# Kernel optimization log

Hardware: AMD Instinct MI355X
Metric: run time of the kernel (lower is better)

The kernel has to match this reference:

```python
import jax, jax.numpy as jnp
import numpy as np

D_MODEL = 512  # scale uses sqrt(d_model), faithful to source (not sqrt(d_k))


def setup_inputs() -> dict:
    key = jax.random.key(0)
    ks = jax.random.split(key, 9)
    S, H, DK, DV = 4096, 8, 128, 64
    w = lambda k, shape: jax.random.normal(k, shape, jnp.float32) * 0.02
    return {
        "x": jax.random.normal(ks[0], (S, D_MODEL), jnp.float32),
        "Wq": w(ks[1], (H, D_MODEL, DK)), "bq": w(ks[2], (H, DK)),
        "Wk": w(ks[3], (H, D_MODEL, DK)), "bk": w(ks[4], (H, DK)),
        "Wv": w(ks[5], (H, D_MODEL, DV)), "bv": w(ks[6], (H, DV)),
        "Wo": w(ks[7], (H * DV, D_MODEL)), "bo": w(ks[8], (D_MODEL,)),
    }


def reference(x, Wq, bq, Wk, bk, Wv, bv, Wo, bo):
    # Per-head Q/K/V projections, batched over heads: [H, S, dk/dv]
    q = jnp.einsum('sd,hdk->hsk', x, Wq) + bq[:, None, :]
    k = jnp.einsum('sd,hdk->hsk', x, Wk) + bk[:, None, :]
    v = jnp.einsum('sd,hdv->hsv', x, Wv) + bv[:, None, :]
    # scaled dot-product; source divides by sqrt(d_model), mask branch is a no-op
    scores = jnp.einsum('hsk,htk->hst', q, k) / jnp.sqrt(jnp.float32(D_MODEL))
    probs = jax.nn.softmax(scores, axis=-1)  # softmax(dim=1) on 2D == last axis
    heads = jnp.einsum('hst,htv->hsv', probs, v)          # [H, S, DV]
    concat = jnp.transpose(heads, (1, 0, 2)).reshape(x.shape[0], -1)  # [S, H*DV]
    return concat @ Wo + bo
```

## Files before the change

kernel.cpp:

```cpp
#include <hip/hip_runtime.h>
#include <hip/hip_bf16.h>
#include <math.h>

typedef __bf16 bf16_t;
typedef __bf16 bf16x4 __attribute__((ext_vector_type(4)));
typedef __bf16 bf16x8 __attribute__((ext_vector_type(8)));
typedef float  f32x4  __attribute__((ext_vector_type(4)));

#define LOG2E   1.4426950408889634f
#define QSCALE  0.04419417382415922f
#define QS_TOT  (QSCALE * LOG2E)

static __device__ __forceinline__ f32x4 mfma16(bf16x8 a, bf16x8 b, f32x4 c) {
    return __builtin_amdgcn_mfma_f32_16x16x32_bf16(a, b, c, 0, 0, 0);
}

static __device__ __forceinline__ void gload16(void* lds, const void* g) {
    __builtin_amdgcn_global_load_lds(
        (const __attribute__((address_space(1))) unsigned int*)g,
        (__attribute__((address_space(3))) unsigned int*)lds, 16, 0, 0);
}

__global__ void k_stage_all(const float* __restrict__ x,
                            const float* __restrict__ Wq, const float* __restrict__ Wk,
                            const float* __restrict__ Wv, const float* __restrict__ Wo,
                            const float* __restrict__ bq, const float* __restrict__ bk,
                            const float* __restrict__ bv,
                            bf16_t* __restrict__ xb, bf16_t* __restrict__ Wcat,
                            bf16_t* __restrict__ Wot, float* __restrict__ bcat) {
    __shared__ float tl[64][65];
    int b = blockIdx.x;
    if (b < 2048) {
        int i = (b * 256 + (int)threadIdx.x) * 4;
        f32x4 v = *(const f32x4*)(x + i);
        bf16x4 o;
        o[0] = (bf16_t)v[0]; o[1] = (bf16_t)v[1]; o[2] = (bf16_t)v[2]; o[3] = (bf16_t)v[3];
        *(bf16x4*)(xb + i) = o;
        return;
    }
    if (b < 2432) {
        int bb = b - 2048;
        int p = bb >> 7, bid = bb & 127;
        int h = bid >> 4, rem = bid & 15, dt = rem >> 1, ct = rem & 1;
        if (p == 2 && ct) return;
        int cols = (p == 2) ? 64 : 128;
        const float* src = (p == 0 ? Wq : (p == 1 ? Wk : Wv)) + h * 512 * cols;
        int d0 = dt * 64, c0 = ct * 64;
        int cin = threadIdx.x & 63, rb = threadIdx.x >> 6;
        #pragma unroll
        for (int j = 0; j < 16; j++) {
            int dl = rb * 16 + j;
            tl[dl][cin] = src[(d0 + dl) * cols + c0 + cin];
        }
        __syncthreads();
        float sc = (p == 0) ? QS_TOT : 1.0f;
        int nl = threadIdx.x >> 2, dch = (threadIdx.x & 3) * 16;
        int n = h * 320 + p * 128 + c0 + nl;
        bf16_t* dst = Wcat + n * 512 + d0 + dch;
        #pragma unroll
        for (int e = 0; e < 16; e += 4) {
            bf16x4 o;
            #pragma unroll
            for (int q = 0; q < 4; q++) o[q] = (bf16_t)(tl[dch + e + q][nl] * sc);
            *(bf16x4*)(dst + e) = o;
        }
        return;
    }
    if (b < 2496) {
        int bb = b - 2432;
        int r0 = (bb >> 3) * 64, c0 = (bb & 7) * 64;
        int cin = threadIdx.x & 63, rb = threadIdx.x >> 6;
        #pragma unroll
        for (int j = 0; j < 16; j++) {
            int rl = rb * 16 + j;
            tl[rl][cin] = Wo[(r0 + rl) * 512 + c0 + cin];
        }
        __syncthreads();
        int nl = threadIdx.x >> 2, dch = (threadIdx.x & 3) * 16;
        bf16_t* dst = Wot + (c0 + nl) * 512 + r0 + dch;
        #pragma unroll
        for (int e = 0; e < 16; e += 4) {
            bf16x4 o;
            #pragma unroll
            for (int q = 0; q < 4; q++) o[q] = (bf16_t)tl[dch + e + q][nl];
            *(bf16x4*)(dst + e) = o;
        }
        return;
    }
    {
        int n = (b - 2496) * 256 + (int)threadIdx.x;
        if (n >= 2560) return;
        int h = n / 320, r = n % 320;
        float v;
        if (r < 128)      v = bq[h * 128 + r] * QS_TOT;
        else if (r < 256) v = bk[h * 128 + r - 128];
        else              v = bv[h * 64 + r - 256];
        bcat[n] = v;
    }
}

static __device__ __forceinline__ void stage_tile(bf16_t* lds, const bf16_t* src_base,
                                                  int row0, int kk, int wv, int lane) {
    #pragma unroll
    for (int j = 0; j < 2; ++j) {
        int row = j * 64 + wv * 16 + (lane >> 2);
        int slot = lane & 3;
        const bf16_t* src = src_base + (size_t)(row0 + row) * 512 + kk
                          + ((slot ^ ((row >> 1) & 3)) << 3);
        gload16(lds + (j * 64 + wv * 16) * 32, src);
    }
}

__global__ __launch_bounds__(256) void k_gemm_qkv(
        const bf16_t* __restrict__ xb, const bf16_t* __restrict__ Wcat,
        const float* __restrict__ bcat,
        bf16_t* __restrict__ Qb, bf16_t* __restrict__ Kb, bf16_t* __restrict__ Vt) {
    __shared__ __align__(16) bf16_t a_lds[2][128 * 32];
    __shared__ __align__(16) bf16_t b_lds[2][128 * 32];

    int lane = threadIdx.x & 63, wv = threadIdx.x >> 6;
    int qi = lane & 15, g = lane >> 4;
    int m0 = blockIdx.x * 128;
    int n0 = blockIdx.y * 128;

    f32x4 acc[4][4];
    #pragma unroll
    for (int ar = 0; ar < 4; ar++)
        #pragma unroll
        for (int br = 0; br < 4; br++) acc[ar][br] = (f32x4){0.f,0.f,0.f,0.f};

    int arow0 = (wv >> 1) * 64;
    int brow0 = (wv & 1) * 64;

    stage_tile(&a_lds[0][0], xb,   m0, 0, wv, lane);
    stage_tile(&b_lds[0][0], Wcat, n0, 0, wv, lane);

    for (int t = 0; t < 16; ++t) {
        __syncthreads();
        int cur = t & 1;
        if (t + 1 < 16) {
            stage_tile(&a_lds[cur ^ 1][0], xb,   m0, (t + 1) * 32, wv, lane);
            stage_tile(&b_lds[cur ^ 1][0], Wcat, n0, (t + 1) * 32, wv, lane);
        }
        const char* abase = (const char*)&a_lds[cur][0];
        const char* bbase = (const char*)&b_lds[cur][0];
        bf16x8 af[4], bf[4];
        #pragma unroll
        for (int ar = 0; ar < 4; ar++) {
            int row = arow0 + ar * 16 + qi;
            af[ar] = *(const bf16x8*)(abase + row * 64 + (((g ^ (row >> 1)) & 3) << 4));
        }
        #pragma unroll
        for (int br = 0; br < 4; br++) {
            int row = brow0 + br * 16 + qi;
            bf[br] = *(const bf16x8*)(bbase + row * 64 + (((g ^ (row >> 1)) & 3) << 4));
        }
        __builtin_amdgcn_s_setprio(1);
        #pragma unroll
        for (int ar = 0; ar < 4; ar++)
            #pragma unroll
            for (int br = 0; br < 4; br++)
                acc[ar][br] = mfma16(af[ar], bf[br], acc[ar][br]);
        __builtin_amdgcn_s_setprio(0);
    }

    int mrow = m0 + arow0;
    int ncol = n0 + brow0;
    #pragma unroll
    for (int br = 0; br < 4; br++) {
        int n = ncol + br * 16 + qi;
        float bias = bcat[n];
        int h = n / 320, r = n % 320;
        #pragma unroll
        for (int ar = 0; ar < 4; ar++)
            #pragma unroll
            for (int i = 0; i < 4; i++) {
                int rr = mrow + ar * 16 + g * 4 + i;
                float val = acc[ar][br][i] + bias;
                if (r < 128)      Qb[(h * 4096 + rr) * 128 + r]         = (bf16_t)val;
                else if (r < 256) Kb[(h * 4096 + rr) * 128 + (r - 128)] = (bf16_t)val;
                else {
                    int cp = (rr & ~31) | (((rr >> 2) & 3) << 3) | (((rr >> 4) & 1) << 2) | (rr & 3);
                    Vt[(h * 64 + (r - 256)) * 4096 + cp] = (bf16_t)val;
                }
            }
    }
}

static __device__ __forceinline__ void stage_k(bf16_t* kbuf, const bf16_t* Kh,
                                               int kt, int wv, int lane) {
    #pragma unroll
    for (int j = 0; j < 4; ++j) {
        int local = wv * 16 + j * 4 + (lane >> 4);
        int physcol = (lane & 15) << 4;
        const char* src = (const char*)(Kh + (size_t)(kt + local) * 128)
                        + (physcol ^ ((local & 7) << 4));
        gload16(kbuf + (wv * 16 + j * 4) * 128, src);
    }
}

static __device__ __forceinline__ void stage_v(bf16_t* vbuf, const bf16_t* Vh,
                                               int kt, int wv, int lane) {
    #pragma unroll
    for (int jj = 0; jj < 2; ++jj) {
        int j = wv * 2 + jj;
        int dv = j * 8 + (lane >> 3);
        int slot = lane & 7;
        const bf16_t* src = Vh + (size_t)dv * 4096 + kt + ((slot ^ (dv & 7)) << 3);
        gload16(vbuf + j * 512, src);
    }
}

__global__ __launch_bounds__(256) void k_attn(
        const bf16_t* __restrict__ Qb, const bf16_t* __restrict__ Kb,
        const bf16_t* __restrict__ Vt, bf16_t* __restrict__ Cb,
        float* __restrict__ Opart, float* __restrict__ Lpart) {
    __shared__ __align__(16) bf16_t k_lds[2][64 * 128];
    __shared__ __align__(16) bf16_t v_lds[3][64 * 64];

    const int lane = threadIdx.x & 63, wv = threadIdx.x >> 6;
    const int qi = lane & 15, g = lane >> 4;

    int nwg = 32 * 8 * gridDim.z, cpx = nwg >> 3;
    int wgid = blockIdx.x + 32 * (blockIdx.y + 8 * blockIdx.z);
    int wk = (wgid & 7) * cpx + (wgid >> 3);
    const int qb = wk & 31, h = (wk >> 5) & 7, split = wk >> 8;

    const int nsplits = gridDim.z;
    const int tbase = 64 / nsplits, trem = 64 % nsplits;
    const int tstart = split * tbase + (split < trem ? split : trem);
    const int ntiles = tbase + (split < trem ? 1 : 0);

    const int q0 = qb * 128 + wv * 32;
    int rot = (int)(((unsigned)wgid * 2654435761u) >> 24) % ntiles;

    const bf16_t* Qh = Qb + h * 4096 * 128;
    const bf16_t* Kh = Kb + h * 4096 * 128;
    const bf16_t* Vh = Vt + h * 64 * 4096;

    bf16x8 qf[2][4];
    #pragma unroll
    for (int qt = 0; qt < 2; qt++)
        #pragma unroll
        for (int c = 0; c < 4; c++)
            qf[qt][c] = *(const bf16x8*)(Qh + (q0 + qt * 16 + qi) * 128 + c * 32 + g * 8);

    bf16x8 vones;
    #pragma unroll
    for (int e = 0; e < 8; e++) vones[e] = (bf16_t)1.0f;

    f32x4 oacc[2][4], lacc[2];
    #pragma unroll
    for (int qt = 0; qt < 2; qt++) {
        #pragma unroll
        for (int c = 0; c < 4; c++) oacc[qt][c] = (f32x4){0.f,0.f,0.f,0.f};
        lacc[qt] = (f32x4){0.f,0.f,0.f,0.f};
    }

    bf16x8 pbp[2][2];

    {
        int kt0 = (tstart + rot) * 64;
        stage_k(&k_lds[0][0], Kh, kt0, wv, lane);
        stage_v(&v_lds[0][0], Vh, kt0, wv, lane);
    }
    __syncthreads();

    int bc = 0;
    for (int ii = 0; ii < ntiles; ++ii) {
        const int kcur = ii & 1;
        int bn = bc + 1; if (bn == 3) bn = 0;
        int bp = bn + 1; if (bp == 3) bp = 0;

        if (ii + 1 < ntiles) {
            int idn = ii + 1 + rot; if (idn >= ntiles) idn -= ntiles;
            int ktn = (tstart + idn) * 64;
            stage_k(&k_lds[kcur ^ 1][0], Kh, ktn, wv, lane);
            stage_v(&v_lds[bn][0], Vh, ktn, wv, lane);
        }

        f32x4 s[2][4];
        #pragma unroll
        for (int qt = 0; qt < 2; qt++)
            #pragma unroll
            for (int t = 0; t < 4; t++) s[qt][t] = (f32x4){0.f,0.f,0.f,0.f};
        __builtin_amdgcn_s_setprio(1);
        #pragma unroll
        for (int t = 0; t < 4; t++) {
            const bf16_t* kr = &k_lds[kcur][(t * 16 + qi) * 128];
            #pragma unroll
            for (int c = 0; c < 4; c++) {
                int offb = (c * 64 + g * 16) ^ ((qi & 7) << 4);
                bf16x8 kf = *(const bf16x8*)(kr + (offb >> 1));
                s[0][t] = mfma16(kf, qf[0][c], s[0][t]);
                s[1][t] = mfma16(kf, qf[1][c], s[1][t]);
            }
        }

        if (ii > 0) {
            #pragma unroll
            for (int c = 0; c < 4; c++) {
                const char* vrow = (const char*)&v_lds[bp][0] + (c * 16 + qi) * 128;
                #pragma unroll
                for (int u = 0; u < 2; u++) {
                    int offb = (g * 16 + u * 64) ^ ((qi & 7) << 4);
                    bf16x8 vf = *(const bf16x8*)(vrow + offb);
                    oacc[0][c] = mfma16(vf, pbp[0][u], oacc[0][c]);
                    oacc[1][c] = mfma16(vf, pbp[1][u], oacc[1][c]);
                }
            }
            #pragma unroll
            for (int u = 0; u < 2; u++) {
                lacc[0] = mfma16(vones, pbp[0][u], lacc[0]);
                lacc[1] = mfma16(vones, pbp[1][u], lacc[1]);
            }
        }
        __builtin_amdgcn_s_setprio(0);

        float p[2][4][4];
        #pragma unroll
        for (int qt = 0; qt < 2; qt++)
            #pragma unroll
            for (int t = 0; t < 4; t++)
                #pragma unroll
                for (int i = 0; i < 4; i++)
                    p[qt][t][i] = __builtin_amdgcn_exp2f(s[qt][t][i]);

        #pragma unroll
        for (int qt = 0; qt < 2; qt++)
            #pragma unroll
            for (int u = 0; u < 2; u++) {
                bf16x8 t8;
                #pragma unroll
                for (int e = 0; e < 4; e++) {
                    t8[e]     = (bf16_t)p[qt][2 * u][e];
                    t8[4 + e] = (bf16_t)p[qt][2 * u + 1][e];
                }
                pbp[qt][u] = t8;
            }

        bc = bn;
        __syncthreads();
    }

    {
        int bl = bc + 2; if (bl >= 3) bl -= 3;
        __builtin_amdgcn_s_setprio(1);
        #pragma unroll
        for (int c = 0; c < 4; c++) {
            const char* vrow = (const char*)&v_lds[bl][0] + (c * 16 + qi) * 128;
            #pragma unroll
            for (int u = 0; u < 2; u++) {
                int offb = (g * 16 + u * 64) ^ ((qi & 7) << 4);
                bf16x8 vf = *(const bf16x8*)(vrow + offb);
                oacc[0][c] = mfma16(vf, pbp[0][u], oacc[0][c]);
                oacc[1][c] = mfma16(vf, pbp[1][u], oacc[1][c]);
            }
        }
        #pragma unroll
        for (int u = 0; u < 2; u++) {
            lacc[0] = mfma16(vones, pbp[0][u], lacc[0]);
            lacc[1] = mfma16(vones, pbp[1][u], lacc[1]);
        }
        __builtin_amdgcn_s_setprio(0);
    }

    float l[2] = { lacc[0][0], lacc[1][0] };

    if (gridDim.z == 1) {
        #pragma unroll
        for (int qt = 0; qt < 2; qt++) {
            float inv = 1.0f / l[qt];
            int q = q0 + qt * 16 + qi;
            #pragma unroll
            for (int c = 0; c < 4; c++) {
                bf16x4 o4;
                #pragma unroll
                for (int i = 0; i < 4; i++) o4[i] = (bf16_t)(oacc[qt][c][i] * inv);
                *(bf16x4*)(Cb + q * 512 + h * 64 + c * 16 + g * 4) = o4;
            }
        }
    } else {
        #pragma unroll
        for (int qt = 0; qt < 2; qt++) {
            int q = q0 + qt * 16 + qi;
            float* Op = Opart + ((size_t)(split * 8 + h) * 4096 + q) * 64;
            #pragma unroll
            for (int c = 0; c < 4; c++)
                *(f32x4*)(Op + c * 16 + g * 4) = oacc[qt][c];
            if (g == 0)
                Lpart[(size_t)(split * 8 + h) * 4096 + q] = l[qt];
        }
    }
}

__global__ void k_merge(const float* __restrict__ Opart, const float* __restrict__ Lpart,
                        bf16_t* __restrict__ Cb, int splits) {
    int idx = blockIdx.x * 256 + threadIdx.x;
    int q = idx >> 7, rem = idx & 127;
    int hv4 = rem * 4;
    int h = hv4 >> 6, dv = hv4 & 63;

    f32x4 acc = {0.f, 0.f, 0.f, 0.f};
    float L = 0.f;
    for (int s = 0; s < splits; s++) {
        L += Lpart[(size_t)(s * 8 + h) * 4096 + q];
        f32x4 ov = *(const f32x4*)(Opart + ((size_t)(s * 8 + h) * 4096 + q) * 64 + dv);
        #pragma unroll
        for (int e = 0; e < 4; e++) acc[e] += ov[e];
    }
    float inv = 1.0f / L;
    bf16x4 o4;
    #pragma unroll
    for (int e = 0; e < 4; e++) o4[e] = (bf16_t)(acc[e] * inv);
    *(bf16x4*)(Cb + (size_t)q * 512 + hv4) = o4;
}

__global__ __launch_bounds__(256) void k_gemm_out(
        const bf16_t* __restrict__ Cb, const bf16_t* __restrict__ Wot,
        const float* __restrict__ bo, float* __restrict__ out) {
    __shared__ __align__(16) bf16_t a_lds[2][128 * 32];
    __shared__ __align__(16) bf16_t b_lds[2][128 * 32];

    int lane = threadIdx.x & 63, wv = threadIdx.x >> 6;
    int qi = lane & 15, g = lane >> 4;
    int m0 = blockIdx.x * 128;
    int n0 = blockIdx.y * 128;

    f32x4 acc[4][4];
    #pragma unroll
    for (int ar = 0; ar < 4; ar++)
        #pragma unroll
        for (int br = 0; br < 4; br++) acc[ar][br] = (f32x4){0.f,0.f,0.f,0.f};

    int arow0 = (wv >> 1) * 64;
    int brow0 = (wv & 1) * 64;

    stage_tile(&a_lds[0][0], Cb,  m0, 0, wv, lane);
    stage_tile(&b_lds[0][0], Wot, n0, 0, wv, lane);

    for (int t = 0; t < 16; ++t) {
        __syncthreads();
        int cur = t & 1;
        if (t + 1 < 16) {
            stage_tile(&a_lds[cur ^ 1][0], Cb,  m0, (t + 1) * 32, wv, lane);
            stage_tile(&b_lds[cur ^ 1][0], Wot, n0, (t + 1) * 32, wv, lane);
        }
        const char* abase = (const char*)&a_lds[cur][0];
        const char* bbase = (const char*)&b_lds[cur][0];
        bf16x8 af[4], bf[4];
        #pragma unroll
        for (int ar = 0; ar < 4; ar++) {
            int row = arow0 + ar * 16 + qi;
            af[ar] = *(const bf16x8*)(abase + row * 64 + (((g ^ (row >> 1)) & 3) << 4));
        }
        #pragma unroll
        for (int br = 0; br < 4; br++) {
            int row = brow0 + br * 16 + qi;
            bf[br] = *(const bf16x8*)(bbase + row * 64 + (((g ^ (row >> 1)) & 3) << 4));
        }
        __builtin_amdgcn_s_setprio(1);
        #pragma unroll
        for (int ar = 0; ar < 4; ar++)
            #pragma unroll
            for (int br = 0; br < 4; br++)
                acc[ar][br] = mfma16(af[ar], bf[br], acc[ar][br]);
        __builtin_amdgcn_s_setprio(0);
    }

    int mrow = m0 + arow0;
    int ncol = n0 + brow0;
    #pragma unroll
    for (int br = 0; br < 4; br++) {
        int n = ncol + br * 16 + qi;
        float bias = bo[n];
        #pragma unroll
        for (int ar = 0; ar < 4; ar++)
            #pragma unroll
            for (int i = 0; i < 4; i++)
                out[(mrow + ar * 16 + g * 4 + i) * 512 + n] = acc[ar][br][i] + bias;
    }
}

extern "C" void kernel_launch(void* const* d_in, const int* in_sizes, int n_in,
                              void* d_out, int out_size, void* d_ws, size_t ws_size,
                              hipStream_t stream) {
    const float* x  = (const float*)d_in[0];
    const float* Wq = (const float*)d_in[1];
    const float* bq = (const float*)d_in[2];
    const float* Wk = (const float*)d_in[3];
    const float* bk = (const float*)d_in[4];
    const float* Wv = (const float*)d_in[5];
    const float* bv = (const float*)d_in[6];
    const float* Wo = (const float*)d_in[7];
    const float* bo = (const float*)d_in[8];
    float* out = (float*)d_out;

    char* ws = (char*)d_ws;
    bf16_t* xb    = (bf16_t*)(ws + 0);
    bf16_t* Wcat  = (bf16_t*)(ws + 4194304);
    bf16_t* Qb    = (bf16_t*)(ws + 6815744);
    bf16_t* Kb    = (bf16_t*)(ws + 15204352);
    bf16_t* Vt    = (bf16_t*)(ws + 23592960);
    bf16_t* Cb    = (bf16_t*)(ws + 27787264);
    bf16_t* Wot   = (bf16_t*)(ws + 31981568);
    float*  bcat  = (float*)(ws + 32505856);
    float*  Opart = (float*)(ws + 32516096);
    float*  Lprt  = (float*)(ws + 49293312);
    const size_t NEED2 = 49555456;
    int splits = (ws_size >= NEED2) ? 2 : 1;

    hipLaunchKernelGGL(k_stage_all,  dim3(2506),   dim3(256), 0, stream,
                       x, Wq, Wk, Wv, Wo, bq, bk, bv, xb, Wcat, Wot, bcat);
    hipLaunchKernelGGL(k_gemm_qkv,   dim3(32, 20), dim3(256), 0, stream, xb, Wcat, bcat, Qb, Kb, Vt);
    hipLaunchKernelGGL(k_attn,       dim3(32, 8, splits), dim3(256), 0, stream, Qb, Kb, Vt, Cb, Opart, Lprt);
    if (splits > 1)
        hipLaunchKernelGGL(k_merge,  dim3(2048),   dim3(256), 0, stream, Opart, Lprt, Cb, splits);
    hipLaunchKernelGGL(k_gemm_out,   dim3(32, 4),  dim3(256), 0, stream, Cb, Wot, bo, out);
}
```

Before: 105.7 us.

## Restructure attention loop to defer softmax exp into next iteration with ping-pong score buffers

The main attention loop now keeps raw scores in two alternating register sets (sA/sB) and unrolls by two. The exp2/bf16 conversion of the previous tile's scores moves into the next iteration, after the current QK^T MFMAs and just before the PV MFMAs. This lets transcendental work overlap with MFMA latency, and the compiler can schedule across a static buffer swap. In exchange it holds more fp32 registers live, which may raise register pressure or lower occupancy, and it enlarges the code.

```diff
diff --git a/kernel.cpp b/kernel.cpp
--- a/kernel.cpp
+++ b/kernel.cpp
@@ -211,6 +211,79 @@
     }
 }
 
+#define QK_TILE(KC, S)                                                         \
+    do {                                                                       \
+        _Pragma("unroll")                                                      \
+        for (int qt = 0; qt < 2; qt++)                                         \
+            _Pragma("unroll")                                                  \
+            for (int t = 0; t < 4; t++) S[qt][t] = (f32x4){0.f,0.f,0.f,0.f};   \
+        __builtin_amdgcn_s_setprio(1);                                         \
+        _Pragma("unroll")                                                      \
+        for (int t = 0; t < 4; t++) {                                          \
+            const bf16_t* kr = &k_lds[KC][(t * 16 + qi) * 128];                \
+            _Pragma("unroll")                                                  \
+            for (int c = 0; c < 4; c++) {                                      \
+                int offb = (c * 64 + g * 16) ^ ((qi & 7) << 4);                \
+                bf16x8 kf = *(const bf16x8*)(kr + (offb >> 1));                \
+                S[0][t] = mfma16(kf, qf[0][c], S[0][t]);                       \
+                S[1][t] = mfma16(kf, qf[1][c], S[1][t]);                       \
+            }                                                                  \
+        }                                                                      \
+        __builtin_amdgcn_s_setprio(0);                                         \
+    } while (0)
+
+#define SOFT_PV(SP, BP)                                                        \
+    do {                                                                       \
+        bf16x8 pb[2][2];                                                       \
+        _Pragma("unroll")                                                      \
+        for (int qt = 0; qt < 2; qt++)                                         \
+            _Pragma("unroll")                                                  \
+            for (int u = 0; u < 2; u++) {                                      \
+                bf16x8 t8;                                                     \
+                _Pragma("unroll")                                              \
+                for (int e = 0; e < 4; e++) {                                  \
+                    t8[e]     = (bf16_t)__builtin_amdgcn_exp2f(SP[qt][2*u][e]);\
+                    t8[4 + e] = (bf16_t)__builtin_amdgcn_exp2f(SP[qt][2*u+1][e]);\
+                }                                                              \
+                pb[qt][u] = t8;                                                \
+            }                                                                  \
+        __builtin_amdgcn_s_setprio(1);                                         \
+        _Pragma("unroll")                                                      \
+        for (int c = 0; c < 4; c++) {                                          \
+            const char* vrow = (const char*)&v_lds[BP][0] + (c * 16 + qi) * 128;\
+            _Pragma("unroll")                                                  \
+            for (int u = 0; u < 2; u++) {                                      \
+                int offb = (g * 16 + u * 64) ^ ((qi & 7) << 4);                \
+                bf16x8 vf = *(const bf16x8*)(vrow + offb);                     \
+                oacc[0][c] = mfma16(vf, pb[0][u], oacc[0][c]);                 \
+                oacc[1][c] = mfma16(vf, pb[1][u], oacc[1][c]);                 \
+            }                                                                  \
+        }                                                                      \
+        _Pragma("unroll")                                                      \
+        for (int u = 0; u < 2; u++) {                                          \
+            lacc[0] = mfma16(vones, pb[0][u], lacc[0]);                        \
+            lacc[1] = mfma16(vones, pb[1][u], lacc[1]);                        \
+        }                                                                      \
+        __builtin_amdgcn_s_setprio(0);                                         \
+    } while (0)
+
+#define ATTN_BODY(II, SC, SP)                                                  \
+    do {                                                                       \
+        const int kcur = (II) & 1;                                             \
+        int bn = bc + 1; if (bn == 3) bn = 0;                                  \
+        int bp = bn + 1; if (bp == 3) bp = 0;                                  \
+        if ((II) + 1 < ntiles) {                                               \
+            int idn = (II) + 1 + rot; if (idn >= ntiles) idn -= ntiles;        \
+            int ktn = (tstart + idn) * 64;                                     \
+            stage_k(&k_lds[kcur ^ 1][0], Kh, ktn, wv, lane);                   \
+            stage_v(&v_lds[bn][0], Vh, ktn, wv, lane);                         \
+        }                                                                      \
+        QK_TILE(kcur, SC);                                                     \
+        SOFT_PV(SP, bp);                                                       \
+        bc = bn;                                                               \
+        __syncthreads();                                                       \
+    } while (0)
+
 __global__ __launch_bounds__(256) void k_attn(
         const bf16_t* __restrict__ Qb, const bf16_t* __restrict__ Kb,
         const bf16_t* __restrict__ Vt, bf16_t* __restrict__ Cb,
@@ -257,7 +330,7 @@
         lacc[qt] = (f32x4){0.f,0.f,0.f,0.f};
     }
 
-    bf16x8 pbp[2][2];
+    f32x4 sA[2][4], sB[2][4];
 
     {
         int kt0 = (tstart + rot) * 64;
@@ -265,104 +338,34 @@
         stage_v(&v_lds[0][0], Vh, kt0, wv, lane);
     }
     __syncthreads();
-
     int bc = 0;
-    for (int ii = 0; ii < ntiles; ++ii) {
-        const int kcur = ii & 1;
-        int bn = bc + 1; if (bn == 3) bn = 0;
-        int bp = bn + 1; if (bp == 3) bp = 0;
-
-        if (ii + 1 < ntiles) {
-            int idn = ii + 1 + rot; if (idn >= ntiles) idn -= ntiles;
+    {
+        if (ntiles > 1) {
+            int idn = 1 + rot; if (idn >= ntiles) idn -= ntiles;
             int ktn = (tstart + idn) * 64;
-            stage_k(&k_lds[kcur ^ 1][0], Kh, ktn, wv, lane);
-            stage_v(&v_lds[bn][0], Vh, ktn, wv, lane);
-        }
-
-        f32x4 s[2][4];
-        #pragma unroll
-        for (int qt = 0; qt < 2; qt++)
-            #pragma unroll
-            for (int t = 0; t < 4; t++) s[qt][t] = (f32x4){0.f,0.f,0.f,0.f};
-        __builtin_amdgcn_s_setprio(1);
-        #pragma unroll
-        for (int t = 0; t < 4; t++) {
-            const bf16_t* kr = &k_lds[kcur][(t * 16 + qi) * 128];
-            #pragma unroll
-            for (int c = 0; c < 4; c++) {
-                int offb = (c * 64 + g * 16) ^ ((qi & 7) << 4);
-                bf16x8 kf = *(const bf16x8*)(kr + (offb >> 1));
-                s[0][t] = mfma16(kf, qf[0][c], s[0][t]);
-                s[1][t] = mfma16(kf, qf[1][c], s[1][t]);
-            }
-        }
-
-        if (ii > 0) {
-            #pragma unroll
-            for (int c = 0; c < 4; c++) {
-                const char* vrow = (const char*)&v_lds[bp][0] + (c * 16 + qi) * 128;
-                #pragma unroll
-                for (int u = 0; u < 2; u++) {
-                    int offb = (g * 16 + u * 64) ^ ((qi & 7) << 4);
-                    bf16x8 vf = *(const bf16x8*)(vrow + offb);
-                    oacc[0][c] = mfma16(vf, pbp[0][u], oacc[0][c]);
-                    oacc[1][c] = mfma16(vf, pbp[1][u], oacc[1][c]);
-                }
-            }
-            #pragma unroll
-            for (int u = 0; u < 2; u++) {
-                lacc[0] = mfma16(vones, pbp[0][u], lacc[0]);
-                lacc[1] = mfma16(vones, pbp[1][u], lacc[1]);
-            }
-        }
-        __builtin_amdgcn_s_setprio(0);
-
-        float p[2][4][4];
-        #pragma unroll
-        for (int qt = 0; qt < 2; qt++)
-            #pragma unroll
-            for (int t = 0; t < 4; t++)
-                #pragma unroll
-                for (int i = 0; i < 4; i++)
-                    p[qt][t][i] = __builtin_amdgcn_exp2f(s[qt][t][i]);
-
-        #pragma unroll
-        for (int qt = 0; qt < 2; qt++)
-            #pragma unroll
-            for (int u = 0; u < 2; u++) {
-                bf16x8 t8;
-                #pragma unroll
-                for (int e = 0; e < 4; e++) {
-                    t8[e]     = (bf16_t)p[qt][2 * u][e];
-                    t8[4 + e] = (bf16_t)p[qt][2 * u + 1][e];
-                }
-                pbp[qt][u] = t8;
-            }
-
-        bc = bn;
+            stage_k(&k_lds[1][0], Kh, ktn, wv, lane);
+            stage_v(&v_lds[1][0], Vh, ktn, wv, lane);
+        }
+        QK_TILE(0, sA);
+        bc = 1;
         __syncthreads();
+    }
+
+    int ii = 1;
+    for (; ii + 1 < ntiles; ii += 2) {
+        ATTN_BODY(ii,     sB, sA);
+        ATTN_BODY(ii + 1, sA, sB);
+    }
+    bool lastInB = false;
+    if (ii < ntiles) {
+        ATTN_BODY(ii, sB, sA);
+        lastInB = true;
     }
 
     {
         int bl = bc + 2; if (bl >= 3) bl -= 3;
-        __builtin_amdgcn_s_setprio(1);
-        #pragma unroll
-        for (int c = 0; c < 4; c++) {
-            const char* vrow = (const char*)&v_lds[bl][0] + (c * 16 + qi) * 128;
-            #pragma unroll
-            for (int u = 0; u < 2; u++) {
-                int offb = (g * 16 + u * 64) ^ ((qi & 7) << 4);
-                bf16x8 vf = *(const bf16x8*)(vrow + offb);
-                oacc[0][c] = mfma16(vf, pbp[0][u], oacc[0][c]);
-                oacc[1][c] = mfma16(vf, pbp[1][u], oacc[1][c]);
-            }
-        }
-        #pragma unroll
-        for (int u = 0; u < 2; u++) {
-            lacc[0] = mfma16(vones, pbp[0][u], lacc[0]);
-            lacc[1] = mfma16(vones, pbp[1][u], lacc[1]);
-        }
-        __builtin_amdgcn_s_setprio(0);
+        if (lastInB) SOFT_PV(sB, bl);
+        else         SOFT_PV(sA, bl);
     }
 
     float l[2] = { lacc[0][0], lacc[1][0] };
```

Result: slower. 124.4 us (+17.6%).
